# Performance work log

Measured on AMD Instinct MI355X. Metric: run time of the kernel, lower is better.

Reference implementation:

```python
import jax, jax.numpy as jnp
import numpy as np
from jax import lax

N, D = 16384, 512
E_SPEC, E_SHARED = 8, 2


def setup_inputs() -> dict:
    key = jax.random.key(0)
    ks = jax.random.split(key, 7)
    return {
        "x": jax.random.normal(ks[0], (N, D), dtype=jnp.float32),
        "spec_router_logits": jax.random.normal(ks[1], (N, E_SPEC), dtype=jnp.float32),
        "shared_router_logits": jax.random.normal(ks[2], (N, E_SHARED), dtype=jnp.float32),
        "spec_W": jax.random.normal(ks[3], (E_SPEC, D, D), dtype=jnp.float32) * 0.02,
        "spec_b": jax.random.normal(ks[4], (E_SPEC, D), dtype=jnp.float32) * 0.02,
        "shared_W": jax.random.normal(ks[5], (E_SHARED, D, D), dtype=jnp.float32) * 0.02,
        "shared_b": jax.random.normal(ks[6], (E_SHARED, D), dtype=jnp.float32) * 0.02,
        "top_k": 2,
    }


def reference(x, spec_router_logits, shared_router_logits, spec_W, spec_b, shared_W, shared_b, top_k):
    n, e_spec = spec_router_logits.shape
    # --- specific experts: top-k routing with renormalized weights ---
    spec_probs = jax.nn.softmax(spec_router_logits, axis=1)          # [N, E_spec]
    topk_w, topk_idx = lax.top_k(spec_probs, top_k)                  # [N, K]
    topk_w = topk_w / (jnp.sum(topk_w, axis=1, keepdims=True) + 1e-6)
    # dense per-token per-expert weight matrix (zero for unselected), matching
    # the original dense mask-accumulate loop
    weights = jnp.zeros((n, e_spec), dtype=spec_probs.dtype)
    weights = weights.at[jnp.arange(n)[:, None], topk_idx].add(topk_w)  # [N, E_spec]
    # dense eval of all specific experts (Linear d->d), then weighted combine
    spec_outs = jnp.einsum('nd,edf->enf', x, spec_W) + spec_b[:, None, :]  # [E,N,D]
    spec_out = jnp.einsum('ne,enf->nf', weights, spec_outs)                # [N,D]
    # --- shared experts: soft combine over softmax probs ---
    shared_probs = jax.nn.softmax(shared_router_logits, axis=1)           # [N, E_shared]
    shared_outs = jnp.einsum('nd,edf->enf', x, shared_W) + shared_b[:, None, :]
    shared_out = jnp.einsum('ne,enf->nf', shared_probs, shared_outs)
    return spec_out + shared_out
```

## Files before the change

### kernel.cpp

```cpp
#include <hip/hip_runtime.h>
#include <stdint.h>

typedef unsigned short ushort_t;
typedef __attribute__((ext_vector_type(8))) short short8;
typedef __attribute__((ext_vector_type(4))) float f32x4;
typedef __attribute__((ext_vector_type(4))) unsigned int u32x4;

#define TOK  16384
#define DIM  512
#define NPAIR 64
#define MAXTILES 156

__device__ __forceinline__ unsigned short f2bf(float f) {
  union { float f; uint32_t u; } v; v.f = f;
  uint32_t u = v.u;
  uint32_t r = (u + 0x7fffu + ((u >> 16) & 1u)) >> 16;
  return (unsigned short)r;
}

__global__ void k_prep(const float* __restrict__ wspec, const float* __restrict__ wsh,
                       ushort_t* __restrict__ wt,
                       const float* __restrict__ sl, const float* __restrict__ shl,
                       float* __restrict__ w4, int* __restrict__ pairid,
                       int* __restrict__ cnt) {
  if (blockIdx.z < 10) {
    __shared__ float t[32][33];
    int e = blockIdx.z;
    const float* src = (e < 8) ? (wspec + e * DIM * DIM) : (wsh + (e - 8) * DIM * DIM);
    int tx = threadIdx.x, ty = threadIdx.y;
    int d = blockIdx.y * 32 + ty, f = blockIdx.x * 32 + tx;
    t[ty][tx] = src[d * DIM + f];
    __syncthreads();
    int fo = blockIdx.x * 32 + ty, dd = blockIdx.y * 32 + tx;
    wt[(size_t)e * DIM * DIM + fo * DIM + dd] = f2bf(t[tx][ty]);
    return;
  }
  int blk = blockIdx.y * 16 + blockIdx.x;
  if (blk >= 16) return;
  __shared__ int h[NPAIR];
  int tid = threadIdx.y * 32 + threadIdx.x;
  int n = blk * 1024 + tid;
  if (tid < NPAIR) h[tid] = 0;
  __syncthreads();
  float l[8];
  float m = -1e30f;
#pragma unroll
  for (int i = 0; i < 8; ++i) { l[i] = sl[n*8 + i]; m = fmaxf(m, l[i]); }
  float s = 0.f;
#pragma unroll
  for (int i = 0; i < 8; ++i) { l[i] = expf(l[i] - m); s += l[i]; }
  float inv = 1.f / s;
#pragma unroll
  for (int i = 0; i < 8; ++i) l[i] *= inv;
  int i1 = 0; float v1 = l[0];
#pragma unroll
  for (int i = 1; i < 8; ++i) if (l[i] > v1) { v1 = l[i]; i1 = i; }
  int i2 = -1; float v2 = -1.f;
#pragma unroll
  for (int i = 0; i < 8; ++i) if (i != i1 && l[i] > v2) { v2 = l[i]; i2 = i; }
  float rs = 1.f / (v1 + v2 + 1e-6f);
  float w1 = v1 * rs, w2 = v2 * rs;
  int pmin, pmax; float wa, wb;
  if (i1 < i2) { pmin = i1; pmax = i2; wa = w1; wb = w2; }
  else         { pmin = i2; pmax = i1; wa = w2; wb = w1; }
  float s0 = shl[n*2], s1 = shl[n*2 + 1];
  float mm = fmaxf(s0, s1);
  float e0 = expf(s0 - mm), e1 = expf(s1 - mm);
  float si = 1.f / (e0 + e1);
  w4[n*4 + 0] = wa;
  w4[n*4 + 1] = wb;
  w4[n*4 + 2] = e0 * si;
  w4[n*4 + 3] = e1 * si;
  int p = pmin * 8 + pmax;
  pairid[n] = p;
  atomicAdd(&h[p], 1);
  __syncthreads();
  if (tid < NPAIR && h[tid]) atomicAdd(&cnt[tid], h[tid]);
}

__global__ void k_scan(const int* __restrict__ cnt, int* __restrict__ off,
                       int* __restrict__ cursor, int* __restrict__ tsinfo,
                       int* __restrict__ tileinfo, ushort_t* __restrict__ idx) {
  int l = threadIdx.x;
  int c = cnt[l];
  int t = (c + 127) >> 7;
  int sc = c, st = t;
#pragma unroll
  for (int d = 1; d < 64; d <<= 1) {
    int vc = __shfl_up(sc, d, 64);
    int vt = __shfl_up(st, d, 64);
    if (l >= d) { sc += vc; st += vt; }
  }
  int offv = sc - c, tsv = st - t;
  off[l] = offv; cursor[l] = offv;
  if (l == 63) tsinfo[64] = st;
  for (int q = 0; q < t; ++q) tileinfo[tsv + q] = (l << 16) | q;
  for (int i = l; i < 128; i += 64) idx[TOK + i] = 0;
}

__global__ void k_fill(const int* __restrict__ pairid, int* __restrict__ cursor,
                       ushort_t* __restrict__ idx) {
  __shared__ int hcnt[NPAIR];
  __shared__ int hbase[NPAIR];
  int tid = threadIdx.x;
  int n = blockIdx.x * 256 + tid;
  if (tid < NPAIR) hcnt[tid] = 0;
  __syncthreads();
  int p = pairid[n];
  int r = atomicAdd(&hcnt[p], 1);
  __syncthreads();
  if (tid < NPAIR && hcnt[tid]) hbase[tid] = atomicAdd(&cursor[tid], hcnt[tid]);
  __syncthreads();
  idx[hbase[p] + r] = (ushort_t)n;
}

__global__ void k_gather(const float* __restrict__ x, const ushort_t* __restrict__ idx,
                         ushort_t* __restrict__ xg) {
  int row = blockIdx.x * 4 + (threadIdx.x >> 6);
  int lane = threadIdx.x & 63;
  int t = (int)idx[row];
  const float* src = x + (size_t)t * DIM + lane * 8;
  f32x4 v0 = *(const f32x4*)src;
  f32x4 v1 = *(const f32x4*)(src + 4);
  u32x4 o;
  o[0] = (uint32_t)f2bf(v0[0]) | ((uint32_t)f2bf(v0[1]) << 16);
  o[1] = (uint32_t)f2bf(v0[2]) | ((uint32_t)f2bf(v0[3]) << 16);
  o[2] = (uint32_t)f2bf(v1[0]) | ((uint32_t)f2bf(v1[1]) << 16);
  o[3] = (uint32_t)f2bf(v1[2]) | ((uint32_t)f2bf(v1[3]) << 16);
  *(u32x4*)(xg + (size_t)row * DIM + lane * 8) = o;
}

__global__ __launch_bounds__(256, 5)
void k_moe(const ushort_t* __restrict__ xg, const ushort_t* __restrict__ wt,
           const float* __restrict__ w4, const ushort_t* __restrict__ idx,
           const int* __restrict__ off, const int* __restrict__ cnt,
           const int* __restrict__ tsinfo, const int* __restrict__ tileinfo,
           const float* __restrict__ bspec, const float* __restrict__ bsh,
           float* __restrict__ out) {
  __shared__ ushort_t aB[8192];
  __shared__ ushort_t bB[4096];
  __shared__ float wLT[4 * 128];
  __shared__ float wRT[4 * 128];
  __shared__ float bL[4 * 64];

  const int tid  = threadIdx.x;
  const int lane = tid & 63;
  const int w    = tid >> 6;
  const int wr   = w >> 1, wc = w & 1;

  int bx  = blockIdx.x;
  int r   = bx >> 3, cdx = bx & 7;
  if (r >= tsinfo[64]) return;
  int info = tileinfo[r];
  int p = info >> 16, tstart = info & 0xffff;
  const int base = off[p] + (tstart << 7);
  int cl = cnt[p] - (tstart << 7); if (cl > 128) cl = 128;
  const int e0 = p >> 3, e1 = p & 7;
  const int tcol = cdx << 6;

  int soffA[4], soffB[2];
#pragma unroll
  for (int q = 0; q < 4; ++q) {
    int pp  = (q << 12) + tid * 16;
    int row = pp >> 7;
    int kb  = (pp & 127) ^ ((row & 7) << 4);
    soffA[q] = row * DIM + (kb >> 1);
    if (q < 2) soffB[q] = soffA[q];
  }
  const ushort_t* aSrc = xg + (size_t)base * DIM;
  const ushort_t* bSrc = wt + (size_t)tcol * DIM;

  for (int i = tid; i < 512; i += 256) {
    int j = i >> 7, rs = i & 127;
    float wa = 1.f, wb = 1.f;
    if (rs < cl) {
      int t = (int)idx[base + rs];
      wa = w4[t * 4 + j];
      wb = w4[t * 4 + ((j + 1) & 3)];
    }
    wLT[i] = wa;
    wRT[i] = wa / wb;
  }
  if (tid < 256) {
    int j = tid >> 6, col = tid & 63;
    int e = (j == 0) ? e0 : (j == 1) ? e1 : (j == 2) ? 8 : 9;
    bL[tid] = (e < 8) ? bspec[e * DIM + tcol + col] : bsh[(e - 8) * DIM + tcol + col];
  }

  int aRd[4][2], bRd[2][2];
#pragma unroll
  for (int i = 0; i < 4; ++i) {
    int row = wr * 64 + i * 16 + (lane & 15);
#pragma unroll
    for (int ksl = 0; ksl < 2; ++ksl) {
      int kb = ((ksl << 6) + ((lane >> 4) << 4)) ^ ((row & 7) << 4);
      aRd[i][ksl] = row * 128 + kb;
    }
  }
#pragma unroll
  for (int i = 0; i < 2; ++i) {
    int col = wc * 32 + i * 16 + (lane & 15);
#pragma unroll
    for (int ksl = 0; ksl < 2; ++ksl) {
      int kb = ((ksl << 6) + ((lane >> 4) << 4)) ^ ((col & 7) << 4);
      bRd[i][ksl] = col * 128 + kb;
    }
  }

  f32x4 acc[4][2];
#pragma unroll
  for (int a = 0; a < 4; ++a)
#pragma unroll
    for (int b = 0; b < 2; ++b) acc[a][b] = (f32x4){0.f, 0.f, 0.f, 0.f};

#pragma unroll 1
  for (int s = 0; s < 32; ++s) {
    int ks = s >> 2, j = s & 3;
    if (j == 0) {
#pragma unroll
      for (int q = 0; q < 4; ++q)
        __builtin_amdgcn_global_load_lds(
            (const __attribute__((address_space(1))) void*)(aSrc + (ks << 6) + soffA[q]),
            (__attribute__((address_space(3))) void*)((char*)aB + (q << 12) + tid * 16),
            16, 0, 0);
    }
    {
      int e = (j == 0) ? e0 : (j == 1) ? e1 : (j == 2) ? 8 : 9;
      const ushort_t* b = bSrc + ((size_t)e << 18) + (ks << 6);
#pragma unroll
      for (int q = 0; q < 2; ++q)
        __builtin_amdgcn_global_load_lds(
            (const __attribute__((address_space(1))) void*)(b + soffB[q]),
            (__attribute__((address_space(3))) void*)((char*)bB + (q << 12) + tid * 16),
            16, 0, 0);
    }
    __syncthreads();

#pragma unroll
    for (int ksl = 0; ksl < 2; ++ksl) {
      u32x4 af[4], bf[2];
#pragma unroll
      for (int i = 0; i < 4; ++i) af[i] = *(const u32x4*)((const char*)aB + aRd[i][ksl]);
#pragma unroll
      for (int i = 0; i < 2; ++i) bf[i] = *(const u32x4*)((const char*)bB + bRd[i][ksl]);
#pragma unroll
      for (int rb = 0; rb < 4; ++rb) {
        short8 a8 = __builtin_bit_cast(short8, af[rb]);
#pragma unroll
        for (int cb = 0; cb < 2; ++cb) {
          short8 b8 = __builtin_bit_cast(short8, bf[cb]);
          acc[rb][cb] = __builtin_amdgcn_mfma_f32_16x16x32_bf16(a8, b8, acc[rb][cb], 0, 0, 0);
        }
      }
    }

    if (s < 31) {
#pragma unroll
      for (int rb = 0; rb < 4; ++rb) {
        int rl = wr * 64 + rb * 16 + ((lane >> 4) << 2);
        f32x4 rv = *(const f32x4*)&wRT[(j << 7) + rl];
#pragma unroll
        for (int cb = 0; cb < 2; ++cb) acc[rb][cb] *= rv;
      }
    }
    __syncthreads();
  }

#pragma unroll
  for (int rb = 0; rb < 4; ++rb) {
    int rl = wr * 64 + rb * 16 + ((lane >> 4) << 2);
    f32x4 wv[4];
#pragma unroll
    for (int j = 0; j < 4; ++j) wv[j] = *(const f32x4*)&wLT[(j << 7) + rl];
    int tok[4]; bool pr[4];
#pragma unroll
    for (int q = 0; q < 4; ++q) {
      int rs = rl + q; pr[q] = rs < cl;
      tok[q] = pr[q] ? (int)idx[base + rs] : 0;
    }
#pragma unroll
    for (int cb = 0; cb < 2; ++cb) {
      int cloc = wc * 32 + cb * 16 + (lane & 15);
      f32x4 v = acc[rb][cb] * wv[3];
#pragma unroll
      for (int j = 0; j < 4; ++j) v += wv[j] * bL[(j << 6) + cloc];
#pragma unroll
      for (int q = 0; q < 4; ++q)
        if (pr[q]) out[(size_t)tok[q] * DIM + tcol + cloc] = v[q];
    }
  }
}

extern "C" void kernel_launch(void* const* d_in, const int* in_sizes, int n_in,
                              void* d_out, int out_size, void* d_ws, size_t ws_size,
                              hipStream_t stream) {
  (void)in_sizes; (void)n_in; (void)out_size; (void)ws_size;
  const float* x   = (const float*)d_in[0];
  const float* srl = (const float*)d_in[1];
  const float* shl = (const float*)d_in[2];
  const float* sW  = (const float*)d_in[3];
  const float* sb  = (const float*)d_in[4];
  const float* hW  = (const float*)d_in[5];
  const float* hb  = (const float*)d_in[6];
  float* out = (float*)d_out;

  char* ws = (char*)d_ws;
  float*    w4     = (float*)ws;     ws += TOK * 4 * 4;
  int*      pairid = (int*)ws;       ws += TOK * 4;
  ushort_t* idx    = (ushort_t*)ws;  ws += (TOK + 128) * 2 + 256;
  int*      cntp   = (int*)ws;       ws += NPAIR * 4;
  int*      offp   = (int*)ws;       ws += NPAIR * 4;
  int*      curp   = (int*)ws;       ws += NPAIR * 4;
  int*      tsp    = (int*)ws;       ws += (NPAIR + 1) * 4;
  int*      tinfo  = (int*)ws;       ws += MAXTILES * 4 + 208;
  ushort_t* xg     = (ushort_t*)ws;  ws += (size_t)(TOK + 128) * DIM * 2;
  ushort_t* wt     = (ushort_t*)ws;

  hipMemsetAsync(cntp, 0, NPAIR * sizeof(int), stream);
  dim3 tb(32, 32, 1), tg(16, 16, 11);
  k_prep<<<tg, tb, 0, stream>>>(sW, hW, wt, srl, shl, w4, pairid, cntp);
  k_scan<<<1, 64, 0, stream>>>(cntp, offp, curp, tsp, tinfo, idx);
  k_fill<<<TOK / 256, 256, 0, stream>>>(pairid, curp, idx);
  k_gather<<<(TOK + 128) / 4, 256, 0, stream>>>(x, idx, xg);
  k_moe<<<MAXTILES * 8, 256, 0, stream>>>(xg, wt, w4, idx, offp, cntp, tsp, tinfo,
                                          sb, hb, out);
}
```

Before: 92.31 us.

## Double-buffer LDS tiles in the MoE GEMM to overlap loads with MFMA

A and B LDS tiles become two-stage ping-pong buffers. The next B slice, and the next A k-slice a step early, are issued right after the loop-top barrier so global-to-LDS copies run while the current stage's MFMAs execute. This removes the second barrier per iteration and the stall from loading right before compute. In exchange, LDS use doubles and launch bounds drop from 5 to 3 blocks per CU, lowering occupancy.

```diff
diff --git a/kernel.cpp b/kernel.cpp
--- a/kernel.cpp
+++ b/kernel.cpp
@@ -130,15 +130,15 @@
   *(u32x4*)(xg + (size_t)row * DIM + lane * 8) = o;
 }
 
-__global__ __launch_bounds__(256, 5)
+__global__ __launch_bounds__(256, 3)
 void k_moe(const ushort_t* __restrict__ xg, const ushort_t* __restrict__ wt,
            const float* __restrict__ w4, const ushort_t* __restrict__ idx,
            const int* __restrict__ off, const int* __restrict__ cnt,
            const int* __restrict__ tsinfo, const int* __restrict__ tileinfo,
            const float* __restrict__ bspec, const float* __restrict__ bsh,
            float* __restrict__ out) {
-  __shared__ ushort_t aB[8192];
-  __shared__ ushort_t bB[4096];
+  __shared__ ushort_t aB[2][8192];
+  __shared__ ushort_t bB[2][4096];
   __shared__ float wLT[4 * 128];
   __shared__ float wRT[4 * 128];
   __shared__ float bL[4 * 64];
@@ -158,17 +158,39 @@
   const int e0 = p >> 3, e1 = p & 7;
   const int tcol = cdx << 6;
 
-  int soffA[4], soffB[2];
+  int soffA[4];
 #pragma unroll
   for (int q = 0; q < 4; ++q) {
     int pp  = (q << 12) + tid * 16;
     int row = pp >> 7;
     int kb  = (pp & 127) ^ ((row & 7) << 4);
     soffA[q] = row * DIM + (kb >> 1);
-    if (q < 2) soffB[q] = soffA[q];
   }
   const ushort_t* aSrc = xg + (size_t)base * DIM;
   const ushort_t* bSrc = wt + (size_t)tcol * DIM;
+
+  auto stageA = [&](int ks) {
+#pragma unroll
+    for (int q = 0; q < 4; ++q)
+      __builtin_amdgcn_global_load_lds(
+          (const __attribute__((address_space(1))) void*)(aSrc + (ks << 6) + soffA[q]),
+          (__attribute__((address_space(3))) void*)((char*)&aB[ks & 1][0] + (q << 12) + tid * 16),
+          16, 0, 0);
+  };
+  auto stageB = [&](int s) {
+    int ks = s >> 2, j = s & 3;
+    int e = (j == 0) ? e0 : (j == 1) ? e1 : (j == 2) ? 8 : 9;
+    const ushort_t* b = bSrc + ((size_t)e << 18) + (ks << 6);
+#pragma unroll
+    for (int q = 0; q < 2; ++q)
+      __builtin_amdgcn_global_load_lds(
+          (const __attribute__((address_space(1))) void*)(b + soffA[q]),
+          (__attribute__((address_space(3))) void*)((char*)&bB[s & 1][0] + (q << 12) + tid * 16),
+          16, 0, 0);
+  };
+
+  stageA(0);
+  stageB(0);
 
   for (int i = tid; i < 512; i += 256) {
     int j = i >> 7, rs = i & 127;
@@ -216,33 +238,19 @@
 #pragma unroll 1
   for (int s = 0; s < 32; ++s) {
     int ks = s >> 2, j = s & 3;
-    if (j == 0) {
-#pragma unroll
-      for (int q = 0; q < 4; ++q)
-        __builtin_amdgcn_global_load_lds(
-            (const __attribute__((address_space(1))) void*)(aSrc + (ks << 6) + soffA[q]),
-            (__attribute__((address_space(3))) void*)((char*)aB + (q << 12) + tid * 16),
-            16, 0, 0);
-    }
-    {
-      int e = (j == 0) ? e0 : (j == 1) ? e1 : (j == 2) ? 8 : 9;
-      const ushort_t* b = bSrc + ((size_t)e << 18) + (ks << 6);
-#pragma unroll
-      for (int q = 0; q < 2; ++q)
-        __builtin_amdgcn_global_load_lds(
-            (const __attribute__((address_space(1))) void*)(b + soffB[q]),
-            (__attribute__((address_space(3))) void*)((char*)bB + (q << 12) + tid * 16),
-            16, 0, 0);
-    }
     __syncthreads();
-
+    if (s < 31) stageB(s + 1);
+    if (j == 1 && ks < 7) stageA(ks + 1);
+
+    const char* ab = (const char*)&aB[ks & 1][0];
+    const char* bb = (const char*)&bB[s & 1][0];
 #pragma unroll
     for (int ksl = 0; ksl < 2; ++ksl) {
       u32x4 af[4], bf[2];
 #pragma unroll
-      for (int i = 0; i < 4; ++i) af[i] = *(const u32x4*)((const char*)aB + aRd[i][ksl]);
-#pragma unroll
-      for (int i = 0; i < 2; ++i) bf[i] = *(const u32x4*)((const char*)bB + bRd[i][ksl]);
+      for (int i = 0; i < 4; ++i) af[i] = *(const u32x4*)(ab + aRd[i][ksl]);
+#pragma unroll
+      for (int i = 0; i < 2; ++i) bf[i] = *(const u32x4*)(bb + bRd[i][ksl]);
 #pragma unroll
       for (int rb = 0; rb < 4; ++rb) {
         short8 a8 = __builtin_bit_cast(short8, af[rb]);
@@ -263,7 +271,6 @@
         for (int cb = 0; cb < 2; ++cb) acc[rb][cb] *= rv;
       }
     }
-    __syncthreads();
   }
 
 #pragma unroll
```

After: 127.7 us. 38.3% more time.

## Load MFMA operands directly from global memory, dropping LDS staging and barriers

Applied to the files above, without the earlier changes.

The GEMM main loop stops staging A and B tiles through LDS with global_load_lds and per-step barriers. Each wave now loads its own bf16 fragments straight from global memory into registers, hoists the A fragments across the four expert passes of a k-slice, and reads biases from global in the epilogue. Launch bounds drop from 5 to 4 waves per EU to leave more registers. This removes barrier and LDS traffic but gives up intra-block sharing, so A and B rows are fetched redundantly per wave through cache, with uncoalesced 16-byte strided loads and no explicit prefetch.

```diff
diff --git a/kernel.cpp b/kernel.cpp
--- a/kernel.cpp
+++ b/kernel.cpp
@@ -130,18 +130,15 @@
   *(u32x4*)(xg + (size_t)row * DIM + lane * 8) = o;
 }
 
-__global__ __launch_bounds__(256, 5)
+__global__ __launch_bounds__(256, 4)
 void k_moe(const ushort_t* __restrict__ xg, const ushort_t* __restrict__ wt,
            const float* __restrict__ w4, const ushort_t* __restrict__ idx,
            const int* __restrict__ off, const int* __restrict__ cnt,
            const int* __restrict__ tsinfo, const int* __restrict__ tileinfo,
            const float* __restrict__ bspec, const float* __restrict__ bsh,
            float* __restrict__ out) {
-  __shared__ ushort_t aB[8192];
-  __shared__ ushort_t bB[4096];
   __shared__ float wLT[4 * 128];
   __shared__ float wRT[4 * 128];
-  __shared__ float bL[4 * 64];
 
   const int tid  = threadIdx.x;
   const int lane = tid & 63;
@@ -158,18 +155,6 @@
   const int e0 = p >> 3, e1 = p & 7;
   const int tcol = cdx << 6;
 
-  int soffA[4], soffB[2];
-#pragma unroll
-  for (int q = 0; q < 4; ++q) {
-    int pp  = (q << 12) + tid * 16;
-    int row = pp >> 7;
-    int kb  = (pp & 127) ^ ((row & 7) << 4);
-    soffA[q] = row * DIM + (kb >> 1);
-    if (q < 2) soffB[q] = soffA[q];
-  }
-  const ushort_t* aSrc = xg + (size_t)base * DIM;
-  const ushort_t* bSrc = wt + (size_t)tcol * DIM;
-
   for (int i = tid; i < 512; i += 256) {
     int j = i >> 7, rs = i & 127;
     float wa = 1.f, wb = 1.f;
@@ -181,31 +166,21 @@
     wLT[i] = wa;
     wRT[i] = wa / wb;
   }
-  if (tid < 256) {
-    int j = tid >> 6, col = tid & 63;
-    int e = (j == 0) ? e0 : (j == 1) ? e1 : (j == 2) ? 8 : 9;
-    bL[tid] = (e < 8) ? bspec[e * DIM + tcol + col] : bsh[(e - 8) * DIM + tcol + col];
-  }
-
-  int aRd[4][2], bRd[2][2];
-#pragma unroll
-  for (int i = 0; i < 4; ++i) {
-    int row = wr * 64 + i * 16 + (lane & 15);
-#pragma unroll
-    for (int ksl = 0; ksl < 2; ++ksl) {
-      int kb = ((ksl << 6) + ((lane >> 4) << 4)) ^ ((row & 7) << 4);
-      aRd[i][ksl] = row * 128 + kb;
-    }
-  }
-#pragma unroll
-  for (int i = 0; i < 2; ++i) {
-    int col = wc * 32 + i * 16 + (lane & 15);
-#pragma unroll
-    for (int ksl = 0; ksl < 2; ++ksl) {
-      int kb = ((ksl << 6) + ((lane >> 4) << 4)) ^ ((col & 7) << 4);
-      bRd[i][ksl] = col * 128 + kb;
-    }
-  }
+  __syncthreads();
+
+  const int klo = (lane >> 4) << 3;
+  const ushort_t* aP[4];
+#pragma unroll
+  for (int rb = 0; rb < 4; ++rb)
+    aP[rb] = xg + (size_t)(base + wr * 64 + rb * 16 + (lane & 15)) * DIM + klo;
+  const ushort_t* bCol = wt + (size_t)(tcol + wc * 32 + (lane & 15)) * DIM + klo;
+  const ushort_t* bP[4];
+  bP[0] = bCol + ((size_t)e0 << 18);
+  bP[1] = bCol + ((size_t)e1 << 18);
+  bP[2] = bCol + ((size_t)8  << 18);
+  bP[3] = bCol + ((size_t)9  << 18);
+
+  const float* wrtP = &wRT[wr * 64 + ((lane >> 4) << 2)];
 
   f32x4 acc[4][2];
 #pragma unroll
@@ -214,56 +189,43 @@
     for (int b = 0; b < 2; ++b) acc[a][b] = (f32x4){0.f, 0.f, 0.f, 0.f};
 
 #pragma unroll 1
-  for (int s = 0; s < 32; ++s) {
-    int ks = s >> 2, j = s & 3;
-    if (j == 0) {
-#pragma unroll
-      for (int q = 0; q < 4; ++q)
-        __builtin_amdgcn_global_load_lds(
-            (const __attribute__((address_space(1))) void*)(aSrc + (ks << 6) + soffA[q]),
-            (__attribute__((address_space(3))) void*)((char*)aB + (q << 12) + tid * 16),
-            16, 0, 0);
-    }
-    {
-      int e = (j == 0) ? e0 : (j == 1) ? e1 : (j == 2) ? 8 : 9;
-      const ushort_t* b = bSrc + ((size_t)e << 18) + (ks << 6);
-#pragma unroll
-      for (int q = 0; q < 2; ++q)
-        __builtin_amdgcn_global_load_lds(
-            (const __attribute__((address_space(1))) void*)(b + soffB[q]),
-            (__attribute__((address_space(3))) void*)((char*)bB + (q << 12) + tid * 16),
-            16, 0, 0);
-    }
-    __syncthreads();
-
-#pragma unroll
-    for (int ksl = 0; ksl < 2; ++ksl) {
-      u32x4 af[4], bf[2];
-#pragma unroll
-      for (int i = 0; i < 4; ++i) af[i] = *(const u32x4*)((const char*)aB + aRd[i][ksl]);
-#pragma unroll
-      for (int i = 0; i < 2; ++i) bf[i] = *(const u32x4*)((const char*)bB + bRd[i][ksl]);
-#pragma unroll
-      for (int rb = 0; rb < 4; ++rb) {
-        short8 a8 = __builtin_bit_cast(short8, af[rb]);
-#pragma unroll
-        for (int cb = 0; cb < 2; ++cb) {
-          short8 b8 = __builtin_bit_cast(short8, bf[cb]);
-          acc[rb][cb] = __builtin_amdgcn_mfma_f32_16x16x32_bf16(a8, b8, acc[rb][cb], 0, 0, 0);
+  for (int ks = 0; ks < 8; ++ks) {
+    const int ko = ks << 6;
+    u32x4 af[4][2];
+#pragma unroll
+    for (int rb = 0; rb < 4; ++rb) {
+      af[rb][0] = *(const u32x4*)(aP[rb] + ko);
+      af[rb][1] = *(const u32x4*)(aP[rb] + ko + 32);
+    }
+#pragma unroll
+    for (int j = 0; j < 4; ++j) {
+      u32x4 bf[2][2];
+#pragma unroll
+      for (int cb = 0; cb < 2; ++cb) {
+        const ushort_t* bp = bP[j] + cb * (16 * DIM) + ko;
+        bf[cb][0] = *(const u32x4*)(bp);
+        bf[cb][1] = *(const u32x4*)(bp + 32);
+      }
+#pragma unroll
+      for (int ksl = 0; ksl < 2; ++ksl)
+#pragma unroll
+        for (int rb = 0; rb < 4; ++rb) {
+          short8 a8 = __builtin_bit_cast(short8, af[rb][ksl]);
+#pragma unroll
+          for (int cb = 0; cb < 2; ++cb) {
+            short8 b8 = __builtin_bit_cast(short8, bf[cb][ksl]);
+            acc[rb][cb] = __builtin_amdgcn_mfma_f32_16x16x32_bf16(a8, b8, acc[rb][cb], 0, 0, 0);
+          }
+        }
+      if (!(ks == 7 && j == 3)) {
+#pragma unroll
+        for (int rb = 0; rb < 4; ++rb) {
+          f32x4 rv = *(const f32x4*)(wrtP + (j << 7) + rb * 16);
+          acc[rb][0] *= rv;
+          acc[rb][1] *= rv;
         }
       }
     }
-
-    if (s < 31) {
-#pragma unroll
-      for (int rb = 0; rb < 4; ++rb) {
-        int rl = wr * 64 + rb * 16 + ((lane >> 4) << 2);
-        f32x4 rv = *(const f32x4*)&wRT[(j << 7) + rl];
-#pragma unroll
-        for (int cb = 0; cb < 2; ++cb) acc[rb][cb] *= rv;
-      }
-    }
-    __syncthreads();
   }
 
 #pragma unroll
@@ -283,7 +245,11 @@
       int cloc = wc * 32 + cb * 16 + (lane & 15);
       f32x4 v = acc[rb][cb] * wv[3];
 #pragma unroll
-      for (int j = 0; j < 4; ++j) v += wv[j] * bL[(j << 6) + cloc];
+      for (int j = 0; j < 4; ++j) {
+        int e = (j == 0) ? e0 : (j == 1) ? e1 : (j == 2) ? 8 : 9;
+        float bj = (e < 8) ? bspec[e * DIM + tcol + cloc] : bsh[(e - 8) * DIM + tcol + cloc];
+        v += wv[j] * bj;
+      }
 #pragma unroll
       for (int q = 0; q < 4; ++q)
         if (pr[q]) out[(size_t)tok[q] * DIM + tcol + cloc] = v[q];
```

Measured after the change: 216.1 us. 2.34x slower.
